# Kernel tuning notes

Hardware: AMD Instinct MI355X
Metric: run time of the kernel (lower is better)

## Reference

```python
import jax, jax.numpy as jnp
import numpy as np

B, S, HID = 2, 2048, 1024
H, D = 16, 64
NUM_BUCKETS, MAX_DIST = 32, 128
NEG_INF = -1e9


def _rel_buckets(rel_pos, num_buckets, max_distance):
    # decoder (unidirectional): only non-positive relative positions valid
    rp = -jnp.minimum(rel_pos, 0)  # [q,k] >= 0
    max_exact = num_buckets // 2
    is_small = rp < max_exact
    safe = jnp.maximum(rp, 1).astype(jnp.float32)
    large = max_exact + (
        jnp.log(safe / max_exact) / np.log(max_distance / max_exact) * (num_buckets - max_exact)
    ).astype(jnp.int32)
    large = jnp.minimum(large, num_buckets - 1)
    return jnp.where(is_small, rp, large)


def _rotate_half(t):
    t1, t2 = jnp.split(t, 2, axis=-1)
    return jnp.concatenate([-t2, t1], axis=-1)


def setup_inputs() -> dict:
    key = jax.random.key(0)
    ks = jax.random.split(key, 6)
    sc = 0.02
    x = jax.random.normal(ks[0], (B, S, HID), jnp.float32)
    Wq = jax.random.normal(ks[1], (HID, H * D), jnp.float32) * sc
    Wk = jax.random.normal(ks[2], (HID, H * D), jnp.float32) * sc
    Wv = jax.random.normal(ks[3], (HID, H * D), jnp.float32) * sc
    Wo = jax.random.normal(ks[4], (H * D, HID), jnp.float32) * sc
    rel_bias = jax.random.normal(ks[5], (NUM_BUCKETS, H), jnp.float32) * sc
    # rotary tables: emb = cat(freqs, freqs), non-interleave layout
    inv_freq = 1.0 / (10000.0 ** (np.arange(0, D, 2, dtype=np.float32) / D))
    freqs = np.arange(S, dtype=np.float32)[:, None] * inv_freq[None, :]  # [S, D/2]
    emb = np.concatenate([freqs, freqs], axis=-1)  # [S, D]
    cos = jnp.asarray(np.cos(emb), jnp.float32)
    sin = jnp.asarray(np.sin(emb), jnp.float32)
    return {"x": x, "Wq": Wq, "Wk": Wk, "Wv": Wv, "Wo": Wo,
            "rel_bias": rel_bias, "cos": cos, "sin": sin}


def reference(x, Wq, Wk, Wv, Wo, rel_bias, cos, sin):
    # QKV projections (weights stored [in, out])
    q = (x @ Wq).reshape(B, S, H, D)
    k = (x @ Wk).reshape(B, S, H, D)
    v = (x @ Wv).reshape(B, S, H, D)
    # RoPE (non-interleave): q*cos + rotate_half(q)*sin, cos/sin broadcast over B,H
    c = cos[None, :, None, :]
    s = sin[None, :, None, :]
    q = q * c + _rotate_half(q) * s
    k = k * c + _rotate_half(k) * s
    # scores [B,H,S,S]
    scores = jnp.einsum("bqhd,bkhd->bhqk", q, k) / np.sqrt(D).astype(np.float32)
    # learned relative-position bucket bias (T5-style, decoder/unidirectional)
    ctx_pos = jnp.arange(S)[:, None]
    mem_pos = jnp.arange(S)[None, :]
    buckets = _rel_buckets(mem_pos - ctx_pos, NUM_BUCKETS, MAX_DIST)  # [S,S]
    bias = rel_bias[buckets]  # [S,S,H]
    scores = scores + jnp.transpose(bias, (2, 0, 1))[None]
    # causal mask (decoder self-attention)
    causal = mem_pos <= ctx_pos  # [S,S]
    scores = jnp.where(causal[None, None], scores, NEG_INF)
    attn = jax.nn.softmax(scores, axis=-1)
    ctx = jnp.einsum("bhqk,bkhd->bqhd", attn, v).reshape(B, S, H * D)
    return ctx @ Wo
```

## Files before the change

### kernel.cpp

```cpp
#include <hip/hip_runtime.h>
#include <hip/hip_bf16.h>
#include <math.h>

#define B_   2
#define S_   2048
#define HID_ 1024
#define H_   16
#define D_   64

typedef __attribute__((ext_vector_type(8))) short bf16x8;
typedef __attribute__((ext_vector_type(4))) short bf16x4;
typedef __attribute__((ext_vector_type(4))) float f32x4;
typedef __attribute__((ext_vector_type(4))) unsigned uint4v;
typedef unsigned short u16;

template<int V> struct IC { static constexpr int val = V; };

static __device__ __forceinline__ u16 f2bf(float f) {
    unsigned u = __builtin_bit_cast(unsigned, f);
    u += 0x7fffu + ((u >> 16) & 1u);
    return (u16)(u >> 16);
}
static __device__ __forceinline__ unsigned cvtpk(float lo, float hi) {
    unsigned r;
    asm("v_cvt_pk_bf16_f32 %0, %1, %2" : "=v"(r) : "v"(lo), "v"(hi));
    return r;
}
static __device__ __forceinline__ int swzK(int row, int colbytes) {
    return row * 128 + (colbytes ^ ((row & 7) << 4));
}
static __device__ __forceinline__ int swzV(int row, int colbytes) {
    return row * 128 + (colbytes ^ ((row & 7) << 4) ^ (((row >> 3) & 1) << 3));
}
static __device__ __forceinline__ void gll16(const void* g, void* l) {
    __builtin_amdgcn_global_load_lds(
        (const __attribute__((address_space(1))) unsigned int*)g,
        (__attribute__((address_space(3))) unsigned int*)l, 16, 0, 0);
}

__global__ __launch_bounds__(256) void convert_x(const float* __restrict__ in,
                                                 u16* __restrict__ out) {
    int i = blockIdx.x * 256 + threadIdx.x;
    float4 f = ((const float4*)in)[i];
    ushort4 u;
    u.x = f2bf(f.x); u.y = f2bf(f.y); u.z = f2bf(f.z); u.w = f2bf(f.w);
    ((ushort4*)out)[i] = u;
}

__global__ __launch_bounds__(256) void transpose_w4(const float* __restrict__ W0,
                                                    const float* __restrict__ W1,
                                                    const float* __restrict__ W2,
                                                    const float* __restrict__ W3,
                                                    u16* __restrict__ o0,
                                                    u16* __restrict__ o1,
                                                    u16* __restrict__ o2,
                                                    u16* __restrict__ o3) {
    __shared__ float tS[32][33];
    const int z = blockIdx.z;
    const float* in = z == 0 ? W0 : z == 1 ? W1 : z == 2 ? W2 : W3;
    u16* out       = z == 0 ? o0 : z == 1 ? o1 : z == 2 ? o2 : o3;
    const int x = threadIdx.x, y = threadIdx.y;
    const int bx = blockIdx.x * 32, by = blockIdx.y * 32;
    #pragma unroll
    for (int j = 0; j < 4; j++)
        tS[y + j * 8][x] = in[(long)(by + y + j * 8) * HID_ + bx + x];
    __syncthreads();
    #pragma unroll
    for (int j = 0; j < 4; j++)
        out[(long)(bx + y + j * 8) * HID_ + by + x] = f2bf(tS[x][y + j * 8]);
}

template<int OUTBF, int ROPE>
__global__ __launch_bounds__(256, 3) void gemm_bf16(const u16* __restrict__ A,
                                                    const u16* __restrict__ Bt,
                                                    u16* __restrict__ outb,
                                                    float* __restrict__ outf,
                                                    const float* __restrict__ cosb,
                                                    const float* __restrict__ sinb,
                                                    int K) {
    __shared__ u16 As[128 * 32];
    __shared__ u16 Bs[128 * 32];
    const int t = threadIdx.x;
    const int lane = t & 63;
    const int w = t >> 6;
    const int qlane = lane & 15, grp = lane >> 4;
    const int m0 = blockIdx.y * 128, n0 = blockIdx.x * 128;
    const int wr = w >> 1, wc = w & 1;

    f32x4 acc[4][4];
    #pragma unroll
    for (int i = 0; i < 4; i++)
        #pragma unroll
        for (int j = 0; j < 4; j++) acc[i][j] = (f32x4){0.f, 0.f, 0.f, 0.f};

    const int srow = (lane >> 2);
    const int scol = (lane & 3) * 8;
    const int nkt = K >> 5;
    for (int kt = 0; kt < nkt; kt++) {
        const int k0 = kt << 5;
        #pragma unroll
        for (int c = 0; c < 2; c++) {
            const int chunk = w * 2 + c;
            const int row = chunk * 16 + srow;
            gll16(A  + (long)(m0 + row) * K + k0 + scol, As + chunk * 512);
            gll16(Bt + (long)(n0 + row) * K + k0 + scol, Bs + chunk * 512);
        }
        __syncthreads();
        bf16x8 af[4], bfr[4];
        #pragma unroll
        for (int i = 0; i < 4; i++) {
            af[i]  = *(const bf16x8*)(As + (wr * 64 + i * 16 + qlane) * 32 + grp * 8);
            bfr[i] = *(const bf16x8*)(Bs + (wc * 64 + i * 16 + qlane) * 32 + grp * 8);
        }
        #pragma unroll
        for (int mf = 0; mf < 4; mf++)
            #pragma unroll
            for (int nf = 0; nf < 4; nf++)
                acc[mf][nf] = __builtin_amdgcn_mfma_f32_16x16x32_bf16(af[mf], bfr[nf], acc[mf][nf], 0, 0, 0);
        __syncthreads();
    }

    const int gnb = n0 + wc * 64;
    #pragma unroll
    for (int mf = 0; mf < 4; mf++) {
        #pragma unroll
        for (int r = 0; r < 4; r++) {
            const int m = m0 + wr * 64 + mf * 16 + grp * 4 + r;
            float a0 = acc[mf][0][r], a1 = acc[mf][1][r];
            float a2 = acc[mf][2][r], a3 = acc[mf][3][r];
            if (ROPE && gnb < 2048) {
                const int s = m & (S_ - 1);
                const float* cr = cosb + s * 64;
                const float* sr = sinb + s * 64;
                float c0 = cr[qlane], c1 = cr[qlane + 16], c2 = cr[qlane + 32], c3 = cr[qlane + 48];
                float z0 = sr[qlane], z1 = sr[qlane + 16], z2 = sr[qlane + 32], z3 = sr[qlane + 48];
                float n0v = a0 * c0 - a2 * z0;
                float n1v = a1 * c1 - a3 * z1;
                float n2v = a2 * c2 + a0 * z2;
                float n3v = a3 * c3 + a1 * z3;
                if (gnb < 1024) {
                    n0v *= 0.125f; n1v *= 0.125f; n2v *= 0.125f; n3v *= 0.125f;
                }
                a0 = n0v; a1 = n1v; a2 = n2v; a3 = n3v;
            }
            if (OUTBF) {
                const float av[4] = {a0, a1, a2, a3};
                #pragma unroll
                for (int nf = 0; nf < 4; nf++) {
                    const int gn = gnb + nf * 16 + qlane;
                    outb[((long)(gn >> 10)) * ((long)4096 * 1024) + (long)m * 1024 + (gn & 1023)]
                        = f2bf(av[nf]);
                }
            } else {
                const float av[4] = {a0, a1, a2, a3};
                #pragma unroll
                for (int nf = 0; nf < 4; nf++)
                    outf[(long)m * 1024 + gnb + nf * 16 + qlane] = av[nf];
            }
        }
    }
}

#define VCOMP(vv, j) ((j) == 0 ? (vv).x : (j) == 1 ? (vv).y : (j) == 2 ? (vv).z : (vv).w)

__global__ __launch_bounds__(256) void attn_mfma(const u16* __restrict__ q,
                                                 const u16* __restrict__ k,
                                                 const u16* __restrict__ v,
                                                 const float* __restrict__ rel_bias,
                                                 u16* __restrict__ ctx) {
    __shared__ __align__(16) unsigned char kS[2][8192];
    __shared__ __align__(16) unsigned char vS[2][8192];
    __shared__ float bb[2][128];

    const int t    = threadIdx.x;
    const int lane = t & 63;
    const int w    = t >> 6;
    const int n    = blockIdx.x;
    const int rnd  = n >> 8;
    int qtv        = (n >> 3) & 31;
    if (rnd & 1) qtv = 31 - qtv;
    const int qt   = qtv;
    const int hb   = (n & 7) + (rnd << 3);
    const int h    = hb & 15, b = hb >> 4;
    const int q0   = qt * 64;
    const int wq   = w * 16;
    const int qlane = lane & 15;
    const int grp   = lane >> 4;

    const int R  = (t >> 4) * 4;
    const int cf = (t & 15) * 4;

    const long bhbase = ((long)b * S_ * H_ + h) * D_;
    const float bfar  = rel_bias[31 * H_ + h];

    bf16x8 qf0, qf1;
    {
        const u16* qrow = q + bhbase + (long)(q0 + wq + qlane) * (H_ * D_);
        qf0 = *(const bf16x8*)(qrow + grp * 8);
        qf1 = *(const bf16x8*)(qrow + 32 + grp * 8);
    }

    f32x4 oacc[4];
    #pragma unroll
    for (int db = 0; db < 4; db++) oacc[db] = (f32x4){0.f, 0.f, 0.f, 0.f};
    float m_run = -1.0e30f, l_run = 0.f;

    ushort4 kreg[4], vreg[4];
    float breg = 0.f;

    auto prefetch = [&](int k0, bool needb) {
        const u16* kp = k + bhbase + (long)(k0 + R) * (H_ * D_) + cf;
        const u16* vp = v + bhbase + (long)(k0 + R) * (H_ * D_) + cf;
        #pragma unroll
        for (int i = 0; i < 4; i++) {
            kreg[i] = *(const ushort4*)(kp + i * (H_ * D_));
            vreg[i] = *(const ushort4*)(vp + i * (H_ * D_));
        }
        if (needb && t < 128) {
            int rp = (q0 - k0) + t - 63;
            float bv = 0.f;
            if (rp >= 0) {
                int bucket;
                if (rp < 16) bucket = rp;
                else {
                    int lg = (int)(logf((float)rp * 0.0625f) * 7.69437361f);
                    bucket = 16 + lg;
                    if (bucket > 31) bucket = 31;
                }
                bv = rel_bias[bucket * H_ + h];
            }
            breg = bv;
        }
    };
    auto writetile = [&](int buf, bool needb) {
        #pragma unroll
        for (int i = 0; i < 4; i++)
            *(ushort4*)(kS[buf] + swzK(R + i, cf * 2)) = kreg[i];
        #pragma unroll
        for (int j = 0; j < 4; j++) {
            ushort4 tc;
            tc.x = VCOMP(vreg[0], j); tc.y = VCOMP(vreg[1], j);
            tc.z = VCOMP(vreg[2], j); tc.w = VCOMP(vreg[3], j);
            *(ushort4*)(vS[buf] + swzV(cf + j, R * 2)) = tc;
        }
        if (needb && t < 128) bb[buf][t] = breg;
    };

    int cur = 0;

    auto tile = [&](int kt, auto mode_tag) {
        constexpr int MODE = decltype(mode_tag)::val;
        const int k0 = kt * 64;
        const bool has_next = kt < qt;
        if (has_next) {
            const int ktn = kt + 1;
            prefetch(k0 + 64, ktn >= qt - 2);
        }

        __builtin_amdgcn_s_setprio(1);
        f32x4 sacc[4];
        #pragma unroll
        for (int kb = 0; kb < 4; kb++) {
            sacc[kb] = (f32x4){0.f, 0.f, 0.f, 0.f};
            bf16x8 kf0 = *(const bf16x8*)(kS[cur] + swzK(kb * 16 + qlane, grp * 16));
            bf16x8 kf1 = *(const bf16x8*)(kS[cur] + swzK(kb * 16 + qlane, 64 + grp * 16));
            sacc[kb] = __builtin_amdgcn_mfma_f32_16x16x32_bf16(kf0, qf0, sacc[kb], 0, 0, 0);
            sacc[kb] = __builtin_amdgcn_mfma_f32_16x16x32_bf16(kf1, qf1, sacc[kb], 0, 0, 0);
        }
        __builtin_amdgcn_s_setprio(0);

        float pv_[4][4];
        float tmax = -1.0e30f;
        #pragma unroll
        for (int kb = 0; kb < 4; kb++) {
            #pragma unroll
            for (int r = 0; r < 4; r++) {
                float s = sacc[kb][r];
                if (MODE >= 1) {
                    const int k_l = kb * 16 + grp * 4 + r;
                    s += bb[cur][wq + qlane - k_l + 63];
                    if (MODE == 2)
                        s = ((k0 + k_l) <= (q0 + wq + qlane)) ? s : -1.0e9f;
                }
                pv_[kb][r] = s;
            }
            tmax = fmaxf(tmax,
                   fmaxf(fmaxf(pv_[kb][0], pv_[kb][1]), fmaxf(pv_[kb][2], pv_[kb][3])));
        }
        tmax = fmaxf(tmax, __shfl_xor(tmax, 16));
        tmax = fmaxf(tmax, __shfl_xor(tmax, 32));

        float bofs = (MODE == 0) ? bfar : 0.f;
        float teff = tmax + bofs;
        float msub;
        if (__all(teff <= m_run + 8.0f)) {
            msub = m_run - bofs;
        } else {
            float mnew = fmaxf(m_run, teff);
            float scale = __expf(m_run - mnew);
            l_run *= scale;
            float scl[4];
            #pragma unroll
            for (int r = 0; r < 4; r++) scl[r] = __shfl(scale, grp * 4 + r, 64);
            #pragma unroll
            for (int db = 0; db < 4; db++)
                #pragma unroll
                for (int r = 0; r < 4; r++) oacc[db][r] *= scl[r];
            m_run = mnew;
            msub = mnew - bofs;
        }

        float tsum = 0.f;
        #pragma unroll
        for (int kb = 0; kb < 4; kb++)
            #pragma unroll
            for (int r = 0; r < 4; r++) {
                float p = __expf(pv_[kb][r] - msub);
                pv_[kb][r] = p;
                tsum += p;
            }
        tsum += __shfl_xor(tsum, 16);
        tsum += __shfl_xor(tsum, 32);
        l_run += tsum;

        bf16x8 pf[2];
        #pragma unroll
        for (int ks = 0; ks < 2; ks++) {
            unsigned u0 = cvtpk(pv_[2 * ks][0], pv_[2 * ks][1]);
            unsigned u1 = cvtpk(pv_[2 * ks][2], pv_[2 * ks][3]);
            unsigned u2 = cvtpk(pv_[2 * ks + 1][0], pv_[2 * ks + 1][1]);
            unsigned u3 = cvtpk(pv_[2 * ks + 1][2], pv_[2 * ks + 1][3]);
            pf[ks] = __builtin_bit_cast(bf16x8, (uint4v){u0, u1, u2, u3});
        }

        __builtin_amdgcn_s_setprio(1);
        #pragma unroll
        for (int db = 0; db < 4; db++) {
            #pragma unroll
            for (int ks = 0; ks < 2; ks++) {
                bf16x4 lo = *(const bf16x4*)(vS[cur] + swzV(db * 16 + qlane, ks * 64 + grp * 8));
                bf16x4 hi = *(const bf16x4*)(vS[cur] + swzV(db * 16 + qlane, ks * 64 + 32 + grp * 8));
                bf16x8 vf = __builtin_shufflevector(lo, hi, 0, 1, 2, 3, 4, 5, 6, 7);
                oacc[db] = __builtin_amdgcn_mfma_f32_16x16x32_bf16(pf[ks], vf, oacc[db], 0, 0, 0);
            }
        }
        __builtin_amdgcn_s_setprio(0);

        if (has_next) writetile(cur ^ 1, (kt + 1) >= qt - 2);
        __syncthreads();
        cur ^= 1;
    };

    prefetch(0, 0 >= qt - 2);
    writetile(0, 0 >= qt - 2);
    __syncthreads();

    for (int kt = 0; kt <= qt - 3; kt++) tile(kt, IC<0>{});
    for (int kt = (qt >= 2 ? qt - 2 : 0); kt < qt; kt++) tile(kt, IC<1>{});
    tile(qt, IC<2>{});

    float inv = 1.0f / l_run;
    float invr[4];
    #pragma unroll
    for (int r = 0; r < 4; r++) invr[r] = __shfl(inv, grp * 4 + r, 64);
    #pragma unroll
    for (int r = 0; r < 4; r++) {
        long qg = q0 + wq + grp * 4 + r;
        u16* dst = ctx + (long)(b * S_ + qg) * HID_ + h * D_ + qlane;
        #pragma unroll
        for (int db = 0; db < 4; db++)
            dst[db * 16] = f2bf(oacc[db][r] * invr[r]);
    }
}

extern "C" void kernel_launch(void* const* d_in, const int* in_sizes, int n_in,
                              void* d_out, int out_size, void* d_ws, size_t ws_size,
                              hipStream_t stream) {
    const float* x    = (const float*)d_in[0];
    const float* Wq   = (const float*)d_in[1];
    const float* Wk   = (const float*)d_in[2];
    const float* Wv   = (const float*)d_in[3];
    const float* Wo   = (const float*)d_in[4];
    const float* rb   = (const float*)d_in[5];
    const float* cosb = (const float*)d_in[6];
    const float* sinb = (const float*)d_in[7];
    float* out = (float*)d_out;

    char* wsb = (char*)d_ws;
    u16* xb    = (u16*)(wsb);
    u16* wqkvT = (u16*)(wsb + (8L  << 20));
    u16* woT   = (u16*)(wsb + (14L << 20));
    u16* qb    = (u16*)(wsb + (16L << 20));
    u16* kb    = (u16*)(wsb + (24L << 20));
    u16* vb    = (u16*)(wsb + (32L << 20));
    u16* ctxb  = (u16*)(wsb + (40L << 20));

    hipLaunchKernelGGL(convert_x, dim3((B_ * S_ * HID_ / 4) / 256), dim3(256), 0, stream, x, xb);
    hipLaunchKernelGGL(transpose_w4, dim3(32, 32, 4), dim3(32, 8), 0, stream,
                       Wq, Wk, Wv, Wo,
                       wqkvT, wqkvT + (1L << 20), wqkvT + (2L << 20), woT);

    hipLaunchKernelGGL((gemm_bf16<1, 1>), dim3(24, 32), dim3(256), 0, stream,
                       xb, wqkvT, qb, (float*)nullptr, cosb, sinb, HID_);
    hipLaunchKernelGGL(attn_mfma, dim3(S_ / 64 * H_ * B_), dim3(256), 0, stream,
                       qb, kb, vb, rb, ctxb);
    hipLaunchKernelGGL((gemm_bf16<0, 0>), dim3(8, 32), dim3(256), 0, stream,
                       ctxb, woT, (u16*)nullptr, out, (const float*)nullptr, (const float*)nullptr, HID_);
}
```

Baseline: 131.8 us.

## Widen attention blocks to 128 queries, use exp2 softmax, split output GEMM

The attention kernel now processes 128 query rows per 512-thread block, so each K/V tile loaded into shared memory is reused by twice as many waves, and the grid is remapped over heads and query tiles. Waves whose rows lie entirely before a key tile skip its compute. The log2(e) factor is folded into the Q scale and the bias so softmax can use exp2 directly, with a larger rescale threshold. K/V staging loads are restructured, and the output projection uses a new 64-wide N tile GEMM to launch more blocks. The costs are larger blocks with lower occupancy flexibility and some per-wave divergence on the diagonal tiles.

```diff
diff --git a/kernel.cpp b/kernel.cpp
--- a/kernel.cpp
+++ b/kernel.cpp
@@ -14,7 +14,7 @@
 typedef __attribute__((ext_vector_type(4))) unsigned uint4v;
 typedef unsigned short u16;
 
-template<int V> struct IC { static constexpr int val = V; };
+#define LOG2E 1.44269504088896f
 
 static __device__ __forceinline__ u16 f2bf(float f) {
     unsigned u = __builtin_bit_cast(unsigned, f);
@@ -70,14 +70,12 @@
         out[(long)(bx + y + j * 8) * HID_ + by + x] = f2bf(tS[x][y + j * 8]);
 }
 
-template<int OUTBF, int ROPE>
-__global__ __launch_bounds__(256, 3) void gemm_bf16(const u16* __restrict__ A,
-                                                    const u16* __restrict__ Bt,
-                                                    u16* __restrict__ outb,
-                                                    float* __restrict__ outf,
-                                                    const float* __restrict__ cosb,
-                                                    const float* __restrict__ sinb,
-                                                    int K) {
+__global__ __launch_bounds__(256, 3) void gemm_qkv(const u16* __restrict__ A,
+                                                   const u16* __restrict__ Bt,
+                                                   u16* __restrict__ outb,
+                                                   const float* __restrict__ cosb,
+                                                   const float* __restrict__ sinb,
+                                                   int K) {
     __shared__ u16 As[128 * 32];
     __shared__ u16 Bs[128 * 32];
     const int t = threadIdx.x;
@@ -128,7 +126,7 @@
             const int m = m0 + wr * 64 + mf * 16 + grp * 4 + r;
             float a0 = acc[mf][0][r], a1 = acc[mf][1][r];
             float a2 = acc[mf][2][r], a3 = acc[mf][3][r];
-            if (ROPE && gnb < 2048) {
+            if (gnb < 2048) {
                 const int s = m & (S_ - 1);
                 const float* cr = cosb + s * 64;
                 const float* sr = sinb + s * 64;
@@ -139,59 +137,108 @@
                 float n2v = a2 * c2 + a0 * z2;
                 float n3v = a3 * c3 + a1 * z3;
                 if (gnb < 1024) {
-                    n0v *= 0.125f; n1v *= 0.125f; n2v *= 0.125f; n3v *= 0.125f;
+                    const float QS = 0.125f * LOG2E;
+                    n0v *= QS; n1v *= QS; n2v *= QS; n3v *= QS;
                 }
                 a0 = n0v; a1 = n1v; a2 = n2v; a3 = n3v;
             }
-            if (OUTBF) {
-                const float av[4] = {a0, a1, a2, a3};
-                #pragma unroll
-                for (int nf = 0; nf < 4; nf++) {
-                    const int gn = gnb + nf * 16 + qlane;
-                    outb[((long)(gn >> 10)) * ((long)4096 * 1024) + (long)m * 1024 + (gn & 1023)]
-                        = f2bf(av[nf]);
-                }
-            } else {
-                const float av[4] = {a0, a1, a2, a3};
-                #pragma unroll
-                for (int nf = 0; nf < 4; nf++)
-                    outf[(long)m * 1024 + gnb + nf * 16 + qlane] = av[nf];
-            }
-        }
-    }
-}
-
-#define VCOMP(vv, j) ((j) == 0 ? (vv).x : (j) == 1 ? (vv).y : (j) == 2 ? (vv).z : (vv).w)
-
-__global__ __launch_bounds__(256) void attn_mfma(const u16* __restrict__ q,
-                                                 const u16* __restrict__ k,
-                                                 const u16* __restrict__ v,
-                                                 const float* __restrict__ rel_bias,
-                                                 u16* __restrict__ ctx) {
+            const float av[4] = {a0, a1, a2, a3};
+            #pragma unroll
+            for (int nf = 0; nf < 4; nf++) {
+                const int gn = gnb + nf * 16 + qlane;
+                outb[((long)(gn >> 10)) * ((long)4096 * 1024) + (long)m * 1024 + (gn & 1023)]
+                    = f2bf(av[nf]);
+            }
+        }
+    }
+}
+
+__global__ __launch_bounds__(256, 3) void gemm_n64(const u16* __restrict__ A,
+                                                   const u16* __restrict__ Bt,
+                                                   float* __restrict__ outf,
+                                                   int K) {
+    __shared__ u16 As[128 * 32];
+    __shared__ u16 Bs[64 * 32];
+    const int t = threadIdx.x;
+    const int lane = t & 63;
+    const int w = t >> 6;
+    const int qlane = lane & 15, grp = lane >> 4;
+    const int m0 = blockIdx.y * 128, n0 = blockIdx.x * 64;
+
+    f32x4 acc[2][4];
+    #pragma unroll
+    for (int i = 0; i < 2; i++)
+        #pragma unroll
+        for (int j = 0; j < 4; j++) acc[i][j] = (f32x4){0.f, 0.f, 0.f, 0.f};
+
+    const int srow = (lane >> 2);
+    const int scol = (lane & 3) * 8;
+    const int nkt = K >> 5;
+    for (int kt = 0; kt < nkt; kt++) {
+        const int k0 = kt << 5;
+        #pragma unroll
+        for (int c = 0; c < 2; c++) {
+            const int chunk = w * 2 + c;
+            const int row = chunk * 16 + srow;
+            gll16(A + (long)(m0 + row) * K + k0 + scol, As + chunk * 512);
+        }
+        gll16(Bt + (long)(n0 + w * 16 + srow) * K + k0 + scol, Bs + w * 512);
+        __syncthreads();
+        bf16x8 af[2], bfr[4];
+        #pragma unroll
+        for (int i = 0; i < 2; i++)
+            af[i] = *(const bf16x8*)(As + (w * 32 + i * 16 + qlane) * 32 + grp * 8);
+        #pragma unroll
+        for (int i = 0; i < 4; i++)
+            bfr[i] = *(const bf16x8*)(Bs + (i * 16 + qlane) * 32 + grp * 8);
+        #pragma unroll
+        for (int mf = 0; mf < 2; mf++)
+            #pragma unroll
+            for (int nf = 0; nf < 4; nf++)
+                acc[mf][nf] = __builtin_amdgcn_mfma_f32_16x16x32_bf16(af[mf], bfr[nf], acc[mf][nf], 0, 0, 0);
+        __syncthreads();
+    }
+
+    #pragma unroll
+    for (int mf = 0; mf < 2; mf++)
+        #pragma unroll
+        for (int r = 0; r < 4; r++) {
+            const int m = m0 + w * 32 + mf * 16 + grp * 4 + r;
+            #pragma unroll
+            for (int nf = 0; nf < 4; nf++)
+                outf[(long)m * 1024 + n0 + nf * 16 + qlane] = acc[mf][nf][r];
+        }
+}
+
+__global__ __launch_bounds__(512, 4) void attn_mfma(const u16* __restrict__ q,
+                                                    const u16* __restrict__ k,
+                                                    const u16* __restrict__ v,
+                                                    const float* __restrict__ rel_bias,
+                                                    u16* __restrict__ ctx) {
     __shared__ __align__(16) unsigned char kS[2][8192];
     __shared__ __align__(16) unsigned char vS[2][8192];
-    __shared__ float bb[2][128];
+    __shared__ float bb[2][192];
 
     const int t    = threadIdx.x;
     const int lane = t & 63;
     const int w    = t >> 6;
     const int n    = blockIdx.x;
-    const int rnd  = n >> 8;
-    int qtv        = (n >> 3) & 31;
-    if (rnd & 1) qtv = 31 - qtv;
-    const int qt   = qtv;
-    const int hb   = (n & 7) + (rnd << 3);
+    const int xcd  = n & 7;
+    const int hbhi = (n >> 7) & 3;
+    int qtb        = (n >> 3) & 15;
+    if (hbhi & 2) qtb = 15 - qtb;
+    const int hb   = xcd + (hbhi << 3);
     const int h    = hb & 15, b = hb >> 4;
-    const int q0   = qt * 64;
+    const int q0   = qtb * 128;
     const int wq   = w * 16;
     const int qlane = lane & 15;
     const int grp   = lane >> 4;
 
-    const int R  = (t >> 4) * 4;
-    const int cf = (t & 15) * 4;
-
     const long bhbase = ((long)b * S_ * H_ + h) * D_;
-    const float bfar  = rel_bias[31 * H_ + h];
+    const float bfar  = rel_bias[31 * H_ + h] * LOG2E;
+
+    const int kr  = t >> 3,        kc  = (t & 7) * 8;
+    const int vrb = (t >> 5) * 4,  vcp = (t & 31) * 2;
 
     bf16x8 qf0, qf1;
     {
@@ -205,19 +252,18 @@
     for (int db = 0; db < 4; db++) oacc[db] = (f32x4){0.f, 0.f, 0.f, 0.f};
     float m_run = -1.0e30f, l_run = 0.f;
 
-    ushort4 kreg[4], vreg[4];
+    bf16x8 kreg;
+    unsigned vreg[4];
     float breg = 0.f;
 
     auto prefetch = [&](int k0, bool needb) {
-        const u16* kp = k + bhbase + (long)(k0 + R) * (H_ * D_) + cf;
-        const u16* vp = v + bhbase + (long)(k0 + R) * (H_ * D_) + cf;
-        #pragma unroll
-        for (int i = 0; i < 4; i++) {
-            kreg[i] = *(const ushort4*)(kp + i * (H_ * D_));
-            vreg[i] = *(const ushort4*)(vp + i * (H_ * D_));
-        }
-        if (needb && t < 128) {
-            int rp = (q0 - k0) + t - 63;
+        kreg = *(const bf16x8*)(k + bhbase + (long)(k0 + kr) * (H_ * D_) + kc);
+        const u16* vp = v + bhbase + (long)(k0 + vrb) * (H_ * D_) + vcp;
+        #pragma unroll
+        for (int i = 0; i < 4; i++)
+            vreg[i] = *(const unsigned*)(vp + (long)i * (H_ * D_));
+        if (needb && t < 192) {
+            int rp = (q0 - 63) + t - k0;
             float bv = 0.f;
             if (rp >= 0) {
                 int bucket;
@@ -227,137 +273,136 @@
                     bucket = 16 + lg;
                     if (bucket > 31) bucket = 31;
                 }
-                bv = rel_bias[bucket * H_ + h];
+                bv = rel_bias[bucket * H_ + h] * LOG2E;
             }
             breg = bv;
         }
     };
     auto writetile = [&](int buf, bool needb) {
-        #pragma unroll
-        for (int i = 0; i < 4; i++)
-            *(ushort4*)(kS[buf] + swzK(R + i, cf * 2)) = kreg[i];
-        #pragma unroll
-        for (int j = 0; j < 4; j++) {
-            ushort4 tc;
-            tc.x = VCOMP(vreg[0], j); tc.y = VCOMP(vreg[1], j);
-            tc.z = VCOMP(vreg[2], j); tc.w = VCOMP(vreg[3], j);
-            *(ushort4*)(vS[buf] + swzV(cf + j, R * 2)) = tc;
-        }
-        if (needb && t < 128) bb[buf][t] = breg;
+        *(bf16x8*)(kS[buf] + swzK(kr, kc * 2)) = kreg;
+        ushort2 a0 = __builtin_bit_cast(ushort2, vreg[0]);
+        ushort2 a1 = __builtin_bit_cast(ushort2, vreg[1]);
+        ushort2 a2 = __builtin_bit_cast(ushort2, vreg[2]);
+        ushort2 a3 = __builtin_bit_cast(ushort2, vreg[3]);
+        ushort4 d0; d0.x = a0.x; d0.y = a1.x; d0.z = a2.x; d0.w = a3.x;
+        ushort4 d1; d1.x = a0.y; d1.y = a1.y; d1.z = a2.y; d1.w = a3.y;
+        *(ushort4*)(vS[buf] + swzV(vcp,     vrb * 2)) = d0;
+        *(ushort4*)(vS[buf] + swzV(vcp + 1, vrb * 2)) = d1;
+        if (needb && t < 192) bb[buf][t] = breg;
     };
 
+    const int NT = 2 * qtb + 2;
+    const bool needb0 = (q0 < 176);
+    prefetch(0, needb0);
+    writetile(0, needb0);
+    __syncthreads();
+
     int cur = 0;
-
-    auto tile = [&](int kt, auto mode_tag) {
-        constexpr int MODE = decltype(mode_tag)::val;
+    for (int kt = 0; kt < NT; kt++) {
         const int k0 = kt * 64;
-        const bool has_next = kt < qt;
-        if (has_next) {
-            const int ktn = kt + 1;
-            prefetch(k0 + 64, ktn >= qt - 2);
-        }
-
-        __builtin_amdgcn_s_setprio(1);
-        f32x4 sacc[4];
-        #pragma unroll
-        for (int kb = 0; kb < 4; kb++) {
-            sacc[kb] = (f32x4){0.f, 0.f, 0.f, 0.f};
-            bf16x8 kf0 = *(const bf16x8*)(kS[cur] + swzK(kb * 16 + qlane, grp * 16));
-            bf16x8 kf1 = *(const bf16x8*)(kS[cur] + swzK(kb * 16 + qlane, 64 + grp * 16));
-            sacc[kb] = __builtin_amdgcn_mfma_f32_16x16x32_bf16(kf0, qf0, sacc[kb], 0, 0, 0);
-            sacc[kb] = __builtin_amdgcn_mfma_f32_16x16x32_bf16(kf1, qf1, sacc[kb], 0, 0, 0);
-        }
-        __builtin_amdgcn_s_setprio(0);
-
-        float pv_[4][4];
-        float tmax = -1.0e30f;
-        #pragma unroll
-        for (int kb = 0; kb < 4; kb++) {
-            #pragma unroll
-            for (int r = 0; r < 4; r++) {
-                float s = sacc[kb][r];
-                if (MODE >= 1) {
-                    const int k_l = kb * 16 + grp * 4 + r;
-                    s += bb[cur][wq + qlane - k_l + 63];
-                    if (MODE == 2)
-                        s = ((k0 + k_l) <= (q0 + wq + qlane)) ? s : -1.0e9f;
+        const bool has_next = (kt + 1) < NT;
+        const bool needb_n  = (q0 - (k0 + 64)) < 176;
+        if (has_next) prefetch(k0 + 64, needb_n);
+
+        const bool skip = k0 > q0 + wq + 15;
+        if (!skip) {
+            const bool use_bias = (q0 + wq - k0) < 176;
+            const bool is_diag  = (k0 + 63) > (q0 + wq);
+
+            __builtin_amdgcn_s_setprio(1);
+            f32x4 sacc[4];
+            #pragma unroll
+            for (int kb = 0; kb < 4; kb++) {
+                sacc[kb] = (f32x4){0.f, 0.f, 0.f, 0.f};
+                bf16x8 kf0 = *(const bf16x8*)(kS[cur] + swzK(kb * 16 + qlane, grp * 16));
+                bf16x8 kf1 = *(const bf16x8*)(kS[cur] + swzK(kb * 16 + qlane, 64 + grp * 16));
+                sacc[kb] = __builtin_amdgcn_mfma_f32_16x16x32_bf16(kf0, qf0, sacc[kb], 0, 0, 0);
+                sacc[kb] = __builtin_amdgcn_mfma_f32_16x16x32_bf16(kf1, qf1, sacc[kb], 0, 0, 0);
+            }
+            __builtin_amdgcn_s_setprio(0);
+
+            float pv_[4][4];
+            float tmax = -1.0e30f;
+            #pragma unroll
+            for (int kb = 0; kb < 4; kb++) {
+                #pragma unroll
+                for (int r = 0; r < 4; r++) {
+                    float s = sacc[kb][r];
+                    if (use_bias) {
+                        const int k_l = kb * 16 + grp * 4 + r;
+                        s += bb[cur][wq + qlane - k_l + 63];
+                        if (is_diag)
+                            s = ((k0 + k_l) <= (q0 + wq + qlane)) ? s : -1.0e9f;
+                    }
+                    pv_[kb][r] = s;
                 }
-                pv_[kb][r] = s;
-            }
-            tmax = fmaxf(tmax,
-                   fmaxf(fmaxf(pv_[kb][0], pv_[kb][1]), fmaxf(pv_[kb][2], pv_[kb][3])));
-        }
-        tmax = fmaxf(tmax, __shfl_xor(tmax, 16));
-        tmax = fmaxf(tmax, __shfl_xor(tmax, 32));
-
-        float bofs = (MODE == 0) ? bfar : 0.f;
-        float teff = tmax + bofs;
-        float msub;
-        if (__all(teff <= m_run + 8.0f)) {
-            msub = m_run - bofs;
-        } else {
-            float mnew = fmaxf(m_run, teff);
-            float scale = __expf(m_run - mnew);
-            l_run *= scale;
-            float scl[4];
-            #pragma unroll
-            for (int r = 0; r < 4; r++) scl[r] = __shfl(scale, grp * 4 + r, 64);
-            #pragma unroll
-            for (int db = 0; db < 4; db++)
+                tmax = fmaxf(tmax,
+                       fmaxf(fmaxf(pv_[kb][0], pv_[kb][1]), fmaxf(pv_[kb][2], pv_[kb][3])));
+            }
+            tmax = fmaxf(tmax, __shfl_xor(tmax, 16));
+            tmax = fmaxf(tmax, __shfl_xor(tmax, 32));
+
+            const float bofs = use_bias ? 0.f : bfar;
+            const float teff = tmax + bofs;
+            float msub;
+            if (__all(teff <= m_run + 11.5f)) {
+                msub = m_run - bofs;
+            } else {
+                float mnew  = fmaxf(m_run, teff);
+                float scale = __builtin_amdgcn_exp2f(m_run - mnew);
+                l_run *= scale;
+                float scl[4];
                 #pragma unroll
-                for (int r = 0; r < 4; r++) oacc[db][r] *= scl[r];
-            m_run = mnew;
-            msub = mnew - bofs;
-        }
-
-        float tsum = 0.f;
-        #pragma unroll
-        for (int kb = 0; kb < 4; kb++)
-            #pragma unroll
-            for (int r = 0; r < 4; r++) {
-                float p = __expf(pv_[kb][r] - msub);
-                pv_[kb][r] = p;
-                tsum += p;
-            }
-        tsum += __shfl_xor(tsum, 16);
-        tsum += __shfl_xor(tsum, 32);
-        l_run += tsum;
-
-        bf16x8 pf[2];
-        #pragma unroll
-        for (int ks = 0; ks < 2; ks++) {
-            unsigned u0 = cvtpk(pv_[2 * ks][0], pv_[2 * ks][1]);
-            unsigned u1 = cvtpk(pv_[2 * ks][2], pv_[2 * ks][3]);
-            unsigned u2 = cvtpk(pv_[2 * ks + 1][0], pv_[2 * ks + 1][1]);
-            unsigned u3 = cvtpk(pv_[2 * ks + 1][2], pv_[2 * ks + 1][3]);
-            pf[ks] = __builtin_bit_cast(bf16x8, (uint4v){u0, u1, u2, u3});
-        }
-
-        __builtin_amdgcn_s_setprio(1);
-        #pragma unroll
-        for (int db = 0; db < 4; db++) {
+                for (int r = 0; r < 4; r++) scl[r] = __shfl(scale, grp * 4 + r, 64);
+                #pragma unroll
+                for (int db = 0; db < 4; db++)
+                    #pragma unroll
+                    for (int r = 0; r < 4; r++) oacc[db][r] *= scl[r];
+                m_run = mnew;
+                msub = mnew - bofs;
+            }
+
+            float tsum = 0.f;
+            #pragma unroll
+            for (int kb = 0; kb < 4; kb++)
+                #pragma unroll
+                for (int r = 0; r < 4; r++) {
+                    float p = __builtin_amdgcn_exp2f(pv_[kb][r] - msub);
+                    pv_[kb][r] = p;
+                    tsum += p;
+                }
+            tsum += __shfl_xor(tsum, 16);
+            tsum += __shfl_xor(tsum, 32);
+            l_run += tsum;
+
+            bf16x8 pf[2];
             #pragma unroll
             for (int ks = 0; ks < 2; ks++) {
-                bf16x4 lo = *(const bf16x4*)(vS[cur] + swzV(db * 16 + qlane, ks * 64 + grp * 8));
-                bf16x4 hi = *(const bf16x4*)(vS[cur] + swzV(db * 16 + qlane, ks * 64 + 32 + grp * 8));
-                bf16x8 vf = __builtin_shufflevector(lo, hi, 0, 1, 2, 3, 4, 5, 6, 7);
-                oacc[db] = __builtin_amdgcn_mfma_f32_16x16x32_bf16(pf[ks], vf, oacc[db], 0, 0, 0);
-            }
-        }
-        __builtin_amdgcn_s_setprio(0);
-
-        if (has_next) writetile(cur ^ 1, (kt + 1) >= qt - 2);
+                unsigned u0 = cvtpk(pv_[2 * ks][0], pv_[2 * ks][1]);
+                unsigned u1 = cvtpk(pv_[2 * ks][2], pv_[2 * ks][3]);
+                unsigned u2 = cvtpk(pv_[2 * ks + 1][0], pv_[2 * ks + 1][1]);
+                unsigned u3 = cvtpk(pv_[2 * ks + 1][2], pv_[2 * ks + 1][3]);
+                pf[ks] = __builtin_bit_cast(bf16x8, (uint4v){u0, u1, u2, u3});
+            }
+
+            __builtin_amdgcn_s_setprio(1);
+            #pragma unroll
+            for (int db = 0; db < 4; db++) {
+                #pragma unroll
+                for (int ks = 0; ks < 2; ks++) {
+                    bf16x4 lo = *(const bf16x4*)(vS[cur] + swzV(db * 16 + qlane, ks * 64 + grp * 8));
+                    bf16x4 hi = *(const bf16x4*)(vS[cur] + swzV(db * 16 + qlane, ks * 64 + 32 + grp * 8));
+                    bf16x8 vf = __builtin_shufflevector(lo, hi, 0, 1, 2, 3, 4, 5, 6, 7);
+                    oacc[db] = __builtin_amdgcn_mfma_f32_16x16x32_bf16(pf[ks], vf, oacc[db], 0, 0, 0);
+                }
+            }
+            __builtin_amdgcn_s_setprio(0);
+        }
+
+        if (has_next) writetile(cur ^ 1, needb_n);
         __syncthreads();
         cur ^= 1;
-    };
-
-    prefetch(0, 0 >= qt - 2);
-    writetile(0, 0 >= qt - 2);
-    __syncthreads();
-
-    for (int kt = 0; kt <= qt - 3; kt++) tile(kt, IC<0>{});
-    for (int kt = (qt >= 2 ? qt - 2 : 0); kt < qt; kt++) tile(kt, IC<1>{});
-    tile(qt, IC<2>{});
+    }
 
     float inv = 1.0f / l_run;
     float invr[4];
@@ -400,10 +445,10 @@
                        Wq, Wk, Wv, Wo,
                        wqkvT, wqkvT + (1L << 20), wqkvT + (2L << 20), woT);
 
-    hipLaunchKernelGGL((gemm_bf16<1, 1>), dim3(24, 32), dim3(256), 0, stream,
-                       xb, wqkvT, qb, (float*)nullptr, cosb, sinb, HID_);
-    hipLaunchKernelGGL(attn_mfma, dim3(S_ / 64 * H_ * B_), dim3(256), 0, stream,
+    hipLaunchKernelGGL(gemm_qkv, dim3(24, 32), dim3(256), 0, stream,
+                       xb, wqkvT, qb, cosb, sinb, HID_);
+    hipLaunchKernelGGL(attn_mfma, dim3(512), dim3(512), 0, stream,
                        qb, kb, vb, rb, ctxb);
-    hipLaunchKernelGGL((gemm_bf16<0, 0>), dim3(8, 32), dim3(256), 0, stream,
-                       ctxb, woT, (u16*)nullptr, out, (const float*)nullptr, (const float*)nullptr, HID_);
-}
+    hipLaunchKernelGGL(gemm_n64, dim3(16, 32), dim3(256), 0, stream,
+                       ctxb, woT, out, HID_);
+}
```

Result: faster. 121.4 us (-7.9%).
